# Optimization experiments

Measured on AMD Instinct MI355X. Metric: run time of the kernel, lower is better.

Reference implementation:

```python
import jax, jax.numpy as jnp
import numpy as np

SPATIAL_SHAPES = [(80, 80), (40, 40), (20, 20)]
NUM_POINTS = [4, 4, 4]
N_HEADS = 8
OFFSET_SCALE = 0.5
LN_EPS = 1e-5


def layer_norm(x, w, b):
    m = x.mean(-1, keepdims=True)
    v = ((x - m) ** 2).mean(-1, keepdims=True)
    return (x - m) * jax.lax.rsqrt(v + LN_EPS) * w + b


def grid_sample(img, grid):
    """Bilinear, zero padding, align_corners=False.
    img: [N, C, H, W], grid: [N, Q, P, 2] in [-1, 1] -> [N, C, Q, P]."""
    N, C, H, W = img.shape
    gx = (grid[..., 0] + 1.0) * (W * 0.5) - 0.5
    gy = (grid[..., 1] + 1.0) * (H * 0.5) - 0.5
    x0 = jnp.floor(gx)
    y0 = jnp.floor(gy)
    wx1 = gx - x0
    wy1 = gy - y0
    x0i = x0.astype(jnp.int32)
    y0i = y0.astype(jnp.int32)
    flat = img.reshape(N, C, H * W)
    Q, P = grid.shape[1], grid.shape[2]

    def corner(xi, yi, w):
        valid = (xi >= 0) & (xi < W) & (yi >= 0) & (yi < H)
        idx = jnp.clip(yi, 0, H - 1) * W + jnp.clip(xi, 0, W - 1)
        v = jnp.take_along_axis(flat, idx.reshape(N, 1, Q * P), axis=2)
        v = v.reshape(N, C, Q, P)
        return v * (w * valid.astype(w.dtype))[:, None]

    return (corner(x0i, y0i, (1 - wx1) * (1 - wy1))
            + corner(x0i + 1, y0i, wx1 * (1 - wy1))
            + corner(x0i, y0i + 1, (1 - wx1) * wy1)
            + corner(x0i + 1, y0i + 1, wx1 * wy1))


def setup_inputs() -> dict:
    key = jax.random.key(0)
    ks = iter(jax.random.split(key, 40))
    B, Q, D, FF = 32, 300, 256, 1024
    S = sum(h * w for h, w in SPATIAL_SHAPES)  # 8400
    SP = sum(NUM_POINTS)  # 12

    def w(shape, scale=0.02):
        return jax.random.normal(next(ks), shape, jnp.float32) * scale

    inp = {
        'hidden_states': jax.random.normal(next(ks), (B, Q, D), jnp.float32),
        'position_embeddings': jax.random.normal(next(ks), (B, Q, D), jnp.float32),
        'reference_points': jax.random.uniform(next(ks), (B, Q, 1, 4), jnp.float32),
        'encoder_hidden_states': jax.random.normal(next(ks), (B, S, D), jnp.float32),
        'q_w': w((D, D)), 'q_b': jnp.zeros((D,), jnp.float32),
        'k_w': w((D, D)), 'k_b': jnp.zeros((D,), jnp.float32),
        'v_w': w((D, D)), 'v_b': jnp.zeros((D,), jnp.float32),
        'o_w': w((D, D)), 'o_b': jnp.zeros((D,), jnp.float32),
        'sa_ln_w': jnp.ones((D,), jnp.float32), 'sa_ln_b': jnp.zeros((D,), jnp.float32),
        'off_w': w((D, N_HEADS * SP * 2)), 'off_b': w((N_HEADS * SP * 2,), 0.1),
        'aw_w': w((D, N_HEADS * SP)), 'aw_b': jnp.zeros((N_HEADS * SP,), jnp.float32),
        'gate_w': w((2 * D, 2 * D)), 'gate_b': jnp.zeros((2 * D,), jnp.float32),
        'gate_ln_w': jnp.ones((D,), jnp.float32), 'gate_ln_b': jnp.zeros((D,), jnp.float32),
        'fc1_w': w((D, FF)), 'fc1_b': jnp.zeros((FF,), jnp.float32),
        'fc2_w': w((FF, D)), 'fc2_b': jnp.zeros((D,), jnp.float32),
        'fin_ln_w': jnp.ones((D,), jnp.float32), 'fin_ln_b': jnp.zeros((D,), jnp.float32),
    }
    return inp


def reference(hidden_states, position_embeddings, reference_points, encoder_hidden_states,
              q_w, q_b, k_w, k_b, v_w, v_b, o_w, o_b, sa_ln_w, sa_ln_b,
              off_w, off_b, aw_w, aw_b, gate_w, gate_b, gate_ln_w, gate_ln_b,
              fc1_w, fc1_b, fc2_w, fc2_b, fin_ln_w, fin_ln_b):
    B, Q, D = hidden_states.shape
    H = N_HEADS
    hd = D // H
    scaling = hd ** -0.5

    # ---- self attention (queries attend to queries, pos added to q/k only) ----
    hq = hidden_states + position_embeddings
    q = ((hq @ q_w + q_b) * scaling).reshape(B, Q, H, hd)
    k = (hq @ k_w + k_b).reshape(B, Q, H, hd)
    v = (hidden_states @ v_w + v_b).reshape(B, Q, H, hd)
    attn = jax.nn.softmax(jnp.einsum('bqhd,bkhd->bhqk', q, k), axis=-1)
    sa = jnp.einsum('bhqk,bkhd->bqhd', attn, v).reshape(B, Q, D) @ o_w + o_b
    hidden_states = layer_norm(hidden_states + sa, sa_ln_w, sa_ln_b)
    second_residual = hidden_states

    # ---- multi-scale deformable cross attention ----
    S = encoder_hidden_states.shape[1]
    SP = sum(NUM_POINTS)
    value = encoder_hidden_states.reshape(B, S, H, hd)
    offs = (hidden_states @ off_w + off_b).reshape(B, Q, H, SP, 2)
    aw = jax.nn.softmax((hidden_states @ aw_w + aw_b).reshape(B, Q, H, SP), axis=-1)
    nps = jnp.asarray([1.0 / n for n in NUM_POINTS for _ in range(n)], hidden_states.dtype)
    offset = offs * nps[:, None] * reference_points[:, :, None, :, 2:] * OFFSET_SCALE
    loc = reference_points[:, :, None, :, :2] + offset          # [B,Q,H,SP,2]
    grids = (2.0 * loc - 1.0).transpose(0, 2, 1, 3, 4).reshape(B * H, Q, SP, 2)
    val = value.transpose(0, 2, 3, 1).reshape(B * H, hd, S)

    sampled = []
    s0, p0 = 0, 0
    for (hl, wl), pl in zip(SPATIAL_SHAPES, NUM_POINTS):
        v_l = val[:, :, s0:s0 + hl * wl].reshape(B * H, hd, hl, wl)
        sampled.append(grid_sample(v_l, grids[:, :, p0:p0 + pl]))
        s0 += hl * wl
        p0 += pl
    sampled = jnp.concatenate(sampled, axis=-1)                 # [B*H,hd,Q,SP]
    aw = aw.transpose(0, 2, 1, 3).reshape(B * H, 1, Q, SP)
    ca = (sampled * aw).sum(-1).reshape(B, D, Q).transpose(0, 2, 1)

    # ---- gated residual ----
    gates = jax.nn.sigmoid(jnp.concatenate([second_residual, ca], -1) @ gate_w + gate_b)
    g1, g2 = gates[..., :D], gates[..., D:]
    hidden_states = layer_norm(g1 * second_residual + g2 * ca, gate_ln_w, gate_ln_b)

    # ---- FFN ----
    ffn = jax.nn.relu(hidden_states @ fc1_w + fc1_b) @ fc2_w + fc2_b
    return layer_norm(hidden_states + ffn, fin_ln_w, fin_ln_b)
```

## Files before the change

kernel.cpp:

```cpp
#include <hip/hip_runtime.h>
#include <cmath>

#define BQ 300
#define DIM 256
#define NH 8
#define HD 32
#define NB 32
#define MROWS 9600
#define SENC 8400

typedef unsigned short ushort_t;
typedef __attribute__((ext_vector_type(8))) short short8;
typedef __attribute__((ext_vector_type(4))) float f32x4;
typedef __attribute__((ext_vector_type(4))) unsigned short us4;

__device__ __forceinline__ float bf2f(ushort_t u) {
    union { unsigned u32; float f; } x; x.u32 = ((unsigned)u) << 16; return x.f;
}
__device__ __forceinline__ ushort_t f2bf(float f) {
    union { float f; unsigned u; } x; x.f = f;
    unsigned u = x.u;
    u += 0x7fffu + ((u >> 16) & 1u);
    return (ushort_t)(u >> 16);
}

__global__ __launch_bounds__(256)
void wtrans_all(const float* __restrict__ q_w, const float* __restrict__ k_w,
                const float* __restrict__ v_w, const float* __restrict__ o_w,
                const float* __restrict__ off_w, const float* __restrict__ aw_w,
                const float* __restrict__ gate_w, const float* __restrict__ fc1_w,
                const float* __restrict__ fc2_w,
                ushort_t* __restrict__ qkT, ushort_t* __restrict__ vT,
                ushort_t* __restrict__ oT, ushort_t* __restrict__ offawT,
                ushort_t* __restrict__ gT, ushort_t* __restrict__ f1T,
                ushort_t* __restrict__ f2T,
                const float* __restrict__ q_b, float* __restrict__ qsb,
                float scal)
{
    __shared__ float t[32][33];
    const int bid = blockIdx.x;
    const float* src; ushort_t* dst; int K, N, local; float scale = 1.0f;

    if (bid < 64)       { src = q_w;   dst = qkT;             K = 256; N = 256;  local = bid;       scale = scal; }
    else if (bid < 128) { src = k_w;   dst = qkT + 256 * 256; K = 256; N = 256;  local = bid - 64; }
    else if (bid < 192) { src = v_w;   dst = vT;              K = 256; N = 256;  local = bid - 128; }
    else if (bid < 256) { src = o_w;   dst = oT;              K = 256; N = 256;  local = bid - 192; }
    else if (bid < 304) { src = off_w; dst = offawT;          K = 256; N = 192;  local = bid - 256; }
    else if (bid < 328) { src = aw_w;  dst = offawT + 192 * 256; K = 256; N = 96; local = bid - 304; }
    else if (bid < 336) {
        int l = bid - 328;
        ushort_t* d2 = offawT + 288 * 256 + l * 32;
        for (int e = threadIdx.x; e < 32 * 32; e += 256) { int r = e >> 5, c = e & 31; d2[r * 256 + c] = 0; }
        return;
    }
    else if (bid < 592) { src = gate_w; dst = gT;  K = 512;  N = 512;  local = bid - 336; }
    else if (bid < 848) { src = fc1_w;  dst = f1T; K = 256;  N = 1024; local = bid - 592; }
    else if (bid < 1104){ src = fc2_w;  dst = f2T; K = 1024; N = 256;  local = bid - 848; }
    else {
        if (threadIdx.x < 256) qsb[threadIdx.x] = q_b[threadIdx.x] * scal;
        return;
    }
    const int tilesx = N >> 5;
    const int n0 = (local % tilesx) * 32, k0 = (local / tilesx) * 32;
    const int tx = threadIdx.x & 31, ty = threadIdx.x >> 5;
    #pragma unroll
    for (int i = 0; i < 4; ++i)
        t[ty + i * 8][tx] = src[(size_t)(k0 + ty + i * 8) * N + n0 + tx];
    __syncthreads();
    #pragma unroll
    for (int i = 0; i < 4; ++i)
        dst[(size_t)(n0 + ty + i * 8) * K + k0 + tx] = f2bf(t[tx][ty + i * 8] * scale);
}

__global__ __launch_bounds__(256)
void cvt2(const float* __restrict__ hidden, const float* __restrict__ pos,
          ushort_t* __restrict__ hq, ushort_t* __restrict__ hid)
{
    int i = blockIdx.x * 256 + threadIdx.x;
    if (i < 614400) {
        float4 a = ((const float4*)hidden)[i];
        float4 b = ((const float4*)pos)[i];
        us4 u;
        u.x = f2bf(a.x + b.x); u.y = f2bf(a.y + b.y);
        u.z = f2bf(a.z + b.z); u.w = f2bf(a.w + b.w);
        *(us4*)&hq[(size_t)i * 4] = u;
    } else {
        i -= 614400;
        float4 a = ((const float4*)hidden)[i];
        us4 u;
        u.x = f2bf(a.x); u.y = f2bf(a.y); u.z = f2bf(a.z); u.w = f2bf(a.w);
        *(us4*)&hid[(size_t)i * 4] = u;
    }
}

template<int BM, int BN, int ACT, bool OBF>
__global__ __launch_bounds__(256)
void gemm_mfma(const ushort_t* __restrict__ A, int lda,
               const ushort_t* __restrict__ Bt, int K,
               const float* __restrict__ bias, const float* __restrict__ bias2,
               int bsplit, int N,
               float* __restrict__ Cf, ushort_t* __restrict__ Cb, int ldc)
{
    constexpr int LDT = 40;
    __shared__ ushort_t As[BM * LDT];
    __shared__ ushort_t Bs[BN * LDT];
    const int tid = threadIdx.x;
    const int row0 = blockIdx.y * BM, col0 = blockIdx.x * BN;
    const int lane = tid & 63, wid = tid >> 6;
    const int wm = wid >> 1, wn = wid & 1;
    constexpr int FM = BM / 32, FN = BN / 32;
    const int r16 = lane & 15, kg = lane >> 4;

    f32x4 acc[FM][FN];
    #pragma unroll
    for (int m = 0; m < FM; ++m)
        #pragma unroll
        for (int n = 0; n < FN; ++n) {
            f32x4 z = {0.f, 0.f, 0.f, 0.f};
            acc[m][n] = z;
        }

    for (int k0 = 0; k0 < K; k0 += 32) {
        #pragma unroll
        for (int c = 0; c < BM * 4 / 256; ++c) {
            int idx = tid + c * 256;
            int r = idx >> 2, cc = idx & 3;
            *(short8*)&As[r * LDT + cc * 8] =
                *(const short8*)&A[(size_t)(row0 + r) * lda + k0 + cc * 8];
        }
        #pragma unroll
        for (int c = 0; c < BN * 4 / 256; ++c) {
            int idx = tid + c * 256;
            int r = idx >> 2, cc = idx & 3;
            *(short8*)&Bs[r * LDT + cc * 8] =
                *(const short8*)&Bt[(size_t)(col0 + r) * K + k0 + cc * 8];
        }
        __syncthreads();
        short8 a[FM], b[FN];
        #pragma unroll
        for (int m = 0; m < FM; ++m)
            a[m] = *(const short8*)&As[(wm * (BM / 2) + m * 16 + r16) * LDT + kg * 8];
        #pragma unroll
        for (int n = 0; n < FN; ++n)
            b[n] = *(const short8*)&Bs[(wn * (BN / 2) + n * 16 + r16) * LDT + kg * 8];
        #pragma unroll
        for (int m = 0; m < FM; ++m)
            #pragma unroll
            for (int n = 0; n < FN; ++n)
                acc[m][n] = __builtin_amdgcn_mfma_f32_16x16x32_bf16(a[m], b[n], acc[m][n], 0, 0, 0);
        __syncthreads();
    }

    #pragma unroll
    for (int m = 0; m < FM; ++m) {
        #pragma unroll
        for (int n = 0; n < FN; ++n) {
            int colb = col0 + wn * (BN / 2) + n * 16 + r16;
            float bs;
            if (colb < bsplit) bs = bias[colb];
            else if (colb < N) bs = bias2[colb - bsplit];
            else bs = 0.0f;
            #pragma unroll
            for (int r = 0; r < 4; ++r) {
                int row = row0 + wm * (BM / 2) + m * 16 + kg * 4 + r;
                float v = acc[m][n][r] + bs;
                if (ACT == 1) v = fmaxf(v, 0.0f);
                if (ACT == 2) v = 1.0f / (1.0f + __expf(-v));
                if (OBF) Cb[(size_t)row * ldc + colb] = f2bf(v);
                else     Cf[(size_t)row * ldc + colb] = v;
            }
        }
    }
}

__global__ __launch_bounds__(256)
void attn_flash(const ushort_t* __restrict__ QK, const ushort_t* __restrict__ V,
                ushort_t* __restrict__ O)
{
    __shared__ ushort_t ks[64 * 40];
    __shared__ ushort_t vt[32 * 72];
    __shared__ float    ss[32 * 68];
    __shared__ ushort_t ps[32 * 72];
    __shared__ float    ml[32], ll[32], fl[32];

    const int orig = blockIdx.x;
    const int wg = (orig & 7) * 320 + (orig >> 3);
    const int qc = wg % 10, bh = wg / 10;
    const int b = bh >> 3, h = bh & 7;
    const int q0 = qc * 32;
    const int nq = (BQ - q0 < 32) ? (BQ - q0) : 32;

    const int tid = threadIdx.x;
    const int lane = tid & 63, wid = tid >> 6;
    const int r16 = lane & 15, kg = lane >> 4;
    const int wm = wid >> 1, wn = wid & 1;

    if (tid < 32) { ml[tid] = -1e30f; ll[tid] = 0.f; }

    short8 aq[2];
    #pragma unroll
    for (int rt = 0; rt < 2; ++rt) {
        int qr = q0 + rt * 16 + r16;
        if (qr > BQ - 1) qr = BQ - 1;
        aq[rt] = *(const short8*)&QK[((size_t)(b * BQ + qr)) * 512 + h * 32 + kg * 8];
    }
    f32x4 oacc = {0.f, 0.f, 0.f, 0.f};

    for (int kt = 0; kt < 5; ++kt) {
        __syncthreads();
        {
            int kk = tid >> 2, c8 = (tid & 3) * 8;
            int ki = kt * 64 + kk;
            short8 kv = {0, 0, 0, 0, 0, 0, 0, 0};
            short8 vv = {0, 0, 0, 0, 0, 0, 0, 0};
            if (ki < BQ) {
                kv = *(const short8*)&QK[((size_t)(b * BQ + ki)) * 512 + 256 + h * 32 + c8];
                vv = *(const short8*)&V[((size_t)(b * BQ + ki)) * 256 + h * 32 + c8];
            }
            *(short8*)&ks[kk * 40 + c8] = kv;
            #pragma unroll
            for (int j = 0; j < 8; ++j) vt[(c8 + j) * 72 + kk] = (ushort_t)vv[j];
        }
        __syncthreads();
        {
            short8 bk = *(const short8*)&ks[(wid * 16 + r16) * 40 + kg * 8];
            #pragma unroll
            for (int rt = 0; rt < 2; ++rt) {
                f32x4 sacc = {0.f, 0.f, 0.f, 0.f};
                sacc = __builtin_amdgcn_mfma_f32_16x16x32_bf16(aq[rt], bk, sacc, 0, 0, 0);
                #pragma unroll
                for (int r = 0; r < 4; ++r)
                    ss[(rt * 16 + kg * 4 + r) * 68 + wid * 16 + r16] = sacc[r];
            }
        }
        __syncthreads();
        #pragma unroll
        for (int j = 0; j < 8; ++j) {
            int row = wid * 8 + j;
            float s = ss[row * 68 + lane];
            if (kt * 64 + lane >= BQ) s = -1e30f;
            float tm = s;
            #pragma unroll
            for (int off = 32; off; off >>= 1) tm = fmaxf(tm, __shfl_xor(tm, off));
            float mold = ml[row];
            float mnew = fmaxf(mold, tm);
            float p = __expf(s - mnew);
            float psum = p;
            #pragma unroll
            for (int off = 32; off; off >>= 1) psum += __shfl_xor(psum, off);
            if (lane == 0) {
                float f = __expf(mold - mnew);
                ml[row] = mnew;
                ll[row] = ll[row] * f + psum;
                fl[row] = f;
            }
            ps[row * 72 + lane] = f2bf(p);
        }
        __syncthreads();
        {
            #pragma unroll
            for (int r = 0; r < 4; ++r)
                oacc[r] *= fl[wm * 16 + kg * 4 + r];
            #pragma unroll
            for (int kstep = 0; kstep < 2; ++kstep) {
                short8 pa = *(const short8*)&ps[(wm * 16 + r16) * 72 + kstep * 32 + kg * 8];
                short8 bv = *(const short8*)&vt[(wn * 16 + r16) * 72 + kstep * 32 + kg * 8];
                oacc = __builtin_amdgcn_mfma_f32_16x16x32_bf16(pa, bv, oacc, 0, 0, 0);
            }
        }
    }
    __syncthreads();
    #pragma unroll
    for (int r = 0; r < 4; ++r) {
        int rowl = wm * 16 + kg * 4 + r;
        if (rowl < nq) {
            float v = oacc[r] / ll[rowl];
            O[((size_t)(b * BQ + q0 + rowl)) * 256 + h * 32 + wn * 16 + r16] = f2bf(v);
        }
    }
}

__global__ __launch_bounds__(256)
void ln_add(const float* __restrict__ X, const float* __restrict__ Y,
            const float* __restrict__ w, const float* __restrict__ b,
            float* __restrict__ outf, ushort_t* __restrict__ outbf, int ldbf)
{
    const int row = blockIdx.x * 4 + (threadIdx.x >> 6);
    const int lane = threadIdx.x & 63;
    float v[4];
    #pragma unroll
    for (int i = 0; i < 4; ++i) {
        int c = lane + 64 * i;
        v[i] = X[(size_t)row * DIM + c] + Y[(size_t)row * DIM + c];
    }
    float s = v[0] + v[1] + v[2] + v[3];
    float s2 = v[0]*v[0] + v[1]*v[1] + v[2]*v[2] + v[3]*v[3];
    #pragma unroll
    for (int off = 32; off; off >>= 1) { s += __shfl_xor(s, off); s2 += __shfl_xor(s2, off); }
    const float mean = s * (1.0f / DIM);
    const float var = s2 * (1.0f / DIM) - mean * mean;
    const float inv = rsqrtf(var + 1e-5f);
    #pragma unroll
    for (int i = 0; i < 4; ++i) {
        int c = lane + 64 * i;
        float r = (v[i] - mean) * inv * w[c] + b[c];
        if (outf)  outf[(size_t)row * DIM + c] = r;
        if (outbf) outbf[(size_t)row * ldbf + c] = f2bf(r);
    }
}

__global__ __launch_bounds__(256)
void ln_gate(const ushort_t* __restrict__ C2, const ushort_t* __restrict__ G,
             const float* __restrict__ w, const float* __restrict__ b,
             float* __restrict__ outf, ushort_t* __restrict__ outbf)
{
    const int row = blockIdx.x * 4 + (threadIdx.x >> 6);
    const int lane = threadIdx.x & 63;
    float v[4];
    #pragma unroll
    for (int i = 0; i < 4; ++i) {
        int c = lane + 64 * i;
        float h1 = bf2f(C2[(size_t)row * 512 + c]);
        float ca = bf2f(C2[(size_t)row * 512 + 256 + c]);
        float g1 = bf2f(G[(size_t)row * 512 + c]);
        float g2 = bf2f(G[(size_t)row * 512 + 256 + c]);
        v[i] = g1 * h1 + g2 * ca;
    }
    float s = v[0] + v[1] + v[2] + v[3];
    float s2 = v[0]*v[0] + v[1]*v[1] + v[2]*v[2] + v[3]*v[3];
    #pragma unroll
    for (int off = 32; off; off >>= 1) { s += __shfl_xor(s, off); s2 += __shfl_xor(s2, off); }
    const float mean = s * (1.0f / DIM);
    const float var = s2 * (1.0f / DIM) - mean * mean;
    const float inv = rsqrtf(var + 1e-5f);
    #pragma unroll
    for (int i = 0; i < 4; ++i) {
        int c = lane + 64 * i;
        float r = (v[i] - mean) * inv * w[c] + b[c];
        outf[(size_t)row * DIM + c] = r;
        outbf[(size_t)row * DIM + c] = f2bf(r);
    }
}

__global__ __launch_bounds__(256)
void sample_kernel(const float* __restrict__ enc, const float* __restrict__ offaw,
                   const float* __restrict__ ref, ushort_t* __restrict__ C2out)
{
    __shared__ float sofs[4][320];
    __shared__ float sref[4][4];

    const int orig = blockIdx.x;
    const int blk = (orig & 7) * 300 + (orig >> 3);
    const int b = blk / 75;
    const int q0 = (blk % 75) * 4;
    const int tid = threadIdx.x;
    const int qq = tid >> 6;
    const int h = (tid >> 3) & 7;
    const int d4 = tid & 7;
    const int bq = b * BQ + q0 + qq;

    for (int e = tid; e < 4 * 80; e += 256) {
        int row = e >> 6 >= 0 ? e / 80 : 0, c4 = e % 80;
        row = e / 80;
        ((float4*)&sofs[row][0])[c4] =
            ((const float4*)(offaw + (size_t)(b * BQ + q0 + row) * 320))[c4];
    }
    if (tid < 16)
        sref[tid >> 2][tid & 3] = ref[(size_t)(b * BQ + q0 + (tid >> 2)) * 4 + (tid & 3)];
    __syncthreads();

    const float rx = sref[qq][0], ry = sref[qq][1];
    const float rw = sref[qq][2], rh = sref[qq][3];
    const float* op = &sofs[qq][h * 24];
    const float* ap = &sofs[qq][192 + h * 12];

    float wgt[12];
    float mx = -1e30f;
    #pragma unroll
    for (int j = 0; j < 12; ++j) { wgt[j] = ap[j]; mx = fmaxf(mx, wgt[j]); }
    float sum = 0.0f;
    #pragma unroll
    for (int j = 0; j < 12; ++j) { wgt[j] = __expf(wgt[j] - mx); sum += wgt[j]; }
    const float isum = 1.0f / sum;

    f32x4 acc = {0.f, 0.f, 0.f, 0.f};
    int p = 0;
    #pragma unroll
    for (int l = 0; l < 3; ++l) {
        const int Wl = (l == 0) ? 80 : (l == 1 ? 40 : 20);
        const int Hl = Wl;
        const int soff = (l == 0) ? 0 : (l == 1 ? 6400 : 8000);
        const float* base = enc + ((size_t)(b * SENC + soff)) * DIM + h * HD + d4 * 4;
        #pragma unroll
        for (int pp = 0; pp < 4; ++pp, ++p) {
            const float ox = op[p * 2 + 0], oy = op[p * 2 + 1];
            const float lx = rx + ox * 0.25f * rw * 0.5f;
            const float ly = ry + oy * 0.25f * rh * 0.5f;
            const float gx = lx * (float)Wl - 0.5f;
            const float gy = ly * (float)Hl - 0.5f;
            const float x0f = floorf(gx), y0f = floorf(gy);
            const int x0 = (int)x0f, y0 = (int)y0f;
            const float wx1 = gx - x0f, wy1 = gy - y0f;
            const float wx0 = 1.0f - wx1, wy0 = 1.0f - wy1;
            const bool vx0 = (x0 >= 0) & (x0 < Wl);
            const bool vx1 = (x0 + 1 >= 0) & (x0 + 1 < Wl);
            const bool vy0 = (y0 >= 0) & (y0 < Hl);
            const bool vy1 = (y0 + 1 >= 0) & (y0 + 1 < Hl);
            const int xc0 = min(max(x0, 0), Wl - 1);
            const int xc1 = min(max(x0 + 1, 0), Wl - 1);
            const int yc0 = min(max(y0, 0), Hl - 1);
            const int yc1 = min(max(y0 + 1, 0), Hl - 1);
            const float aw2 = wgt[p] * isum;
            const float w00 = wx0 * wy0 * ((vx0 & vy0) ? aw2 : 0.0f);
            const float w10 = wx1 * wy0 * ((vx1 & vy0) ? aw2 : 0.0f);
            const float w01 = wx0 * wy1 * ((vx0 & vy1) ? aw2 : 0.0f);
            const float w11 = wx1 * wy1 * ((vx1 & vy1) ? aw2 : 0.0f);
            f32x4 c00 = *(const f32x4*)&base[((size_t)(yc0 * Wl + xc0)) * DIM];
            f32x4 c10 = *(const f32x4*)&base[((size_t)(yc0 * Wl + xc1)) * DIM];
            f32x4 c01 = *(const f32x4*)&base[((size_t)(yc1 * Wl + xc0)) * DIM];
            f32x4 c11 = *(const f32x4*)&base[((size_t)(yc1 * Wl + xc1)) * DIM];
            #pragma unroll
            for (int r = 0; r < 4; ++r)
                acc[r] += w00 * c00[r] + w10 * c10[r] + w01 * c01[r] + w11 * c11[r];
        }
    }
    us4 u;
    u.x = f2bf(acc[0]); u.y = f2bf(acc[1]); u.z = f2bf(acc[2]); u.w = f2bf(acc[3]);
    *(us4*)&C2out[(size_t)bq * 512 + 256 + h * HD + d4 * 4] = u;
}

extern "C" void kernel_launch(void* const* d_in, const int* in_sizes, int n_in,
                              void* d_out, int out_size, void* d_ws, size_t ws_size,
                              hipStream_t stream)
{
    (void)in_sizes; (void)n_in; (void)out_size; (void)ws_size;
    const float* hidden   = (const float*)d_in[0];
    const float* pos      = (const float*)d_in[1];
    const float* ref      = (const float*)d_in[2];
    const float* enc      = (const float*)d_in[3];
    const float* q_w      = (const float*)d_in[4];
    const float* q_b      = (const float*)d_in[5];
    const float* k_w      = (const float*)d_in[6];
    const float* k_b      = (const float*)d_in[7];
    const float* v_w      = (const float*)d_in[8];
    const float* v_b      = (const float*)d_in[9];
    const float* o_w      = (const float*)d_in[10];
    const float* o_b      = (const float*)d_in[11];
    const float* sa_ln_w  = (const float*)d_in[12];
    const float* sa_ln_b  = (const float*)d_in[13];
    const float* off_w    = (const float*)d_in[14];
    const float* off_b    = (const float*)d_in[15];
    const float* aw_w     = (const float*)d_in[16];
    const float* aw_b     = (const float*)d_in[17];
    const float* gate_w   = (const float*)d_in[18];
    const float* gate_b   = (const float*)d_in[19];
    const float* gate_ln_w= (const float*)d_in[20];
    const float* gate_ln_b= (const float*)d_in[21];
    const float* fc1_w    = (const float*)d_in[22];
    const float* fc1_b    = (const float*)d_in[23];
    const float* fc2_w    = (const float*)d_in[24];
    const float* fc2_b    = (const float*)d_in[25];
    const float* fin_ln_w = (const float*)d_in[26];
    const float* fin_ln_b = (const float*)d_in[27];
    float* out = (float*)d_out;

    char* wsb = (char*)d_ws;
    ushort_t* hqbf   = (ushort_t*)(wsb + 0);
    ushort_t* hidbf  = (ushort_t*)(wsb + 4915200);
    ushort_t* QKbuf  = (ushort_t*)(wsb + 9830400);
    ushort_t* Vbf    = (ushort_t*)(wsb + 19660800);
    ushort_t* aobf   = (ushort_t*)(wsb + 24576000);
    float*    SA     = (float*)(wsb + 0);
    ushort_t* C2     = (ushort_t*)(wsb + 9830400);
    float*    offaw  = (float*)(wsb + 19660800);
    ushort_t* gatesbf= (ushort_t*)(wsb + 0);
    ushort_t* midbf  = (ushort_t*)(wsb + 19660800);
    float*    ffn    = (float*)(wsb + 0);
    ushort_t* h2bf   = (ushort_t*)(wsb + 39321600);
    ushort_t* qkT    = (ushort_t*)(wsb + 44236800);
    ushort_t* vT     = (ushort_t*)(wsb + 44498944);
    ushort_t* oT     = (ushort_t*)(wsb + 44630016);
    ushort_t* offawT = (ushort_t*)(wsb + 44761088);
    ushort_t* gT     = (ushort_t*)(wsb + 44924928);
    ushort_t* f1T    = (ushort_t*)(wsb + 45449216);
    ushort_t* f2T    = (ushort_t*)(wsb + 45973504);
    float*    qsb    = (float*)(wsb + 46497792);

    const dim3 blk(256);
    const float scal = 0.17677669529663687f;

    wtrans_all<<<dim3(1105), blk, 0, stream>>>(q_w, k_w, v_w, o_w, off_w, aw_w,
                                               gate_w, fc1_w, fc2_w,
                                               qkT, vT, oT, offawT, gT, f1T, f2T,
                                               q_b, qsb, scal);
    cvt2<<<dim3(4800), blk, 0, stream>>>(hidden, pos, hqbf, hidbf);

    gemm_mfma<128,128,0,true><<<dim3(4,75), blk, 0, stream>>>(hqbf, 256, qkT, 256, qsb, k_b, 256, 512, nullptr, QKbuf, 512);
    gemm_mfma<128,128,0,true><<<dim3(2,75), blk, 0, stream>>>(hidbf, 256, vT, 256, v_b, nullptr, 256, 256, nullptr, Vbf, 256);

    attn_flash<<<dim3(2560), blk, 0, stream>>>(QKbuf, Vbf, aobf);

    gemm_mfma<128,128,0,false><<<dim3(2,75), blk, 0, stream>>>(aobf, 256, oT, 256, o_b, nullptr, 256, 256, SA, nullptr, 256);
    ln_add<<<dim3(2400), blk, 0, stream>>>(SA, hidden, sa_ln_w, sa_ln_b, nullptr, C2, 512);

    gemm_mfma<128,64,0,false><<<dim3(5,75), blk, 0, stream>>>(C2, 512, offawT, 256, off_b, aw_b, 192, 288, offaw, nullptr, 320);

    sample_kernel<<<dim3(2400), blk, 0, stream>>>(enc, offaw, ref, C2);

    gemm_mfma<128,128,2,true><<<dim3(4,75), blk, 0, stream>>>(C2, 512, gT, 512, gate_b, nullptr, 512, 512, nullptr, gatesbf, 512);
    ln_gate<<<dim3(2400), blk, 0, stream>>>(C2, gatesbf, gate_ln_w, gate_ln_b, out, h2bf);

    gemm_mfma<128,128,1,true><<<dim3(8,75), blk, 0, stream>>>(h2bf, 256, f1T, 256, fc1_b, nullptr, 1024, 1024, nullptr, midbf, 1024);
    gemm_mfma<128,128,0,false><<<dim3(2,75), blk, 0, stream>>>(midbf, 1024, f2T, 1024, fc2_b, nullptr, 256, 256, ffn, nullptr, 256);
    ln_add<<<dim3(2400), blk, 0, stream>>>(ffn, out, fin_ln_w, fin_ln_b, out, nullptr, 0);
}
```

Before: 269.1 us.

## Enlarge attention query tile to 64 and precompute sampling indices in shared memory

The flash attention kernel now handles 64 queries per block instead of 32. Each wave owns a 16-row query tile and computes scores across all four key sub-tiles, which halves the grid and halves how often K and V are reloaded from global memory. The deformable sampling kernel now computes the softmax, bilinear weights and corner indices once per (query, head, point) into shared memory, then gathers from that table. Previously the softmax and coordinate math was repeated by all 8 lanes that share a head. The trade-off is more shared memory per block in both kernels, with possible occupancy loss, plus an extra barrier in the sampler.

New measurement: 277.9 us. 1.03x slower.

```diff
diff --git a/kernel.cpp b/kernel.cpp
--- a/kernel.cpp
+++ b/kernel.cpp
@@ -179,32 +179,34 @@
 {
     __shared__ ushort_t ks[64 * 40];
     __shared__ ushort_t vt[32 * 72];
-    __shared__ float    ss[32 * 68];
-    __shared__ ushort_t ps[32 * 72];
-    __shared__ float    ml[32], ll[32], fl[32];
+    __shared__ float    ss[64 * 68];
+    __shared__ ushort_t ps[64 * 72];
+    __shared__ float    ml[64], ll[64], fl[64];
 
     const int orig = blockIdx.x;
-    const int wg = (orig & 7) * 320 + (orig >> 3);
-    const int qc = wg % 10, bh = wg / 10;
+    const int wg = (orig & 7) * 160 + (orig >> 3);
+    const int qc = wg % 5, bh = wg / 5;
     const int b = bh >> 3, h = bh & 7;
-    const int q0 = qc * 32;
-    const int nq = (BQ - q0 < 32) ? (BQ - q0) : 32;
+    const int q0 = qc * 64;
+    const int nq = (BQ - q0 < 64) ? (BQ - q0) : 64;
 
     const int tid = threadIdx.x;
     const int lane = tid & 63, wid = tid >> 6;
     const int r16 = lane & 15, kg = lane >> 4;
-    const int wm = wid >> 1, wn = wid & 1;
-
-    if (tid < 32) { ml[tid] = -1e30f; ll[tid] = 0.f; }
-
-    short8 aq[2];
-    #pragma unroll
-    for (int rt = 0; rt < 2; ++rt) {
-        int qr = q0 + rt * 16 + r16;
+
+    if (tid < 64) { ml[tid] = -1e30f; ll[tid] = 0.f; }
+
+    short8 aq;
+    {
+        int qr = q0 + wid * 16 + r16;
         if (qr > BQ - 1) qr = BQ - 1;
-        aq[rt] = *(const short8*)&QK[((size_t)(b * BQ + qr)) * 512 + h * 32 + kg * 8];
-    }
-    f32x4 oacc = {0.f, 0.f, 0.f, 0.f};
+        aq = *(const short8*)&QK[((size_t)(b * BQ + qr)) * 512 + h * 32 + kg * 8];
+    }
+    f32x4 oacc[2];
+    {
+        f32x4 z = {0.f, 0.f, 0.f, 0.f};
+        oacc[0] = z; oacc[1] = z;
+    }
 
     for (int kt = 0; kt < 5; ++kt) {
         __syncthreads();
@@ -222,21 +224,19 @@
             for (int j = 0; j < 8; ++j) vt[(c8 + j) * 72 + kk] = (ushort_t)vv[j];
         }
         __syncthreads();
-        {
-            short8 bk = *(const short8*)&ks[(wid * 16 + r16) * 40 + kg * 8];
-            #pragma unroll
-            for (int rt = 0; rt < 2; ++rt) {
-                f32x4 sacc = {0.f, 0.f, 0.f, 0.f};
-                sacc = __builtin_amdgcn_mfma_f32_16x16x32_bf16(aq[rt], bk, sacc, 0, 0, 0);
-                #pragma unroll
-                for (int r = 0; r < 4; ++r)
-                    ss[(rt * 16 + kg * 4 + r) * 68 + wid * 16 + r16] = sacc[r];
-            }
+        #pragma unroll
+        for (int ktile = 0; ktile < 4; ++ktile) {
+            short8 bk = *(const short8*)&ks[(ktile * 16 + r16) * 40 + kg * 8];
+            f32x4 sacc = {0.f, 0.f, 0.f, 0.f};
+            sacc = __builtin_amdgcn_mfma_f32_16x16x32_bf16(aq, bk, sacc, 0, 0, 0);
+            #pragma unroll
+            for (int r = 0; r < 4; ++r)
+                ss[(wid * 16 + kg * 4 + r) * 68 + ktile * 16 + r16] = sacc[r];
         }
         __syncthreads();
         #pragma unroll
-        for (int j = 0; j < 8; ++j) {
-            int row = wid * 8 + j;
+        for (int j = 0; j < 16; ++j) {
+            int row = wid * 16 + j;
             float s = ss[row * 68 + lane];
             if (kt * 64 + lane >= BQ) s = -1e30f;
             float tm = s;
@@ -259,25 +259,31 @@
         __syncthreads();
         {
             #pragma unroll
-            for (int r = 0; r < 4; ++r)
-                oacc[r] *= fl[wm * 16 + kg * 4 + r];
-            #pragma unroll
-            for (int kstep = 0; kstep < 2; ++kstep) {
-                short8 pa = *(const short8*)&ps[(wm * 16 + r16) * 72 + kstep * 32 + kg * 8];
-                short8 bv = *(const short8*)&vt[(wn * 16 + r16) * 72 + kstep * 32 + kg * 8];
-                oacc = __builtin_amdgcn_mfma_f32_16x16x32_bf16(pa, bv, oacc, 0, 0, 0);
+            for (int r = 0; r < 4; ++r) {
+                float f = fl[wid * 16 + kg * 4 + r];
+                oacc[0][r] *= f; oacc[1][r] *= f;
             }
+            #pragma unroll
+            for (int nt = 0; nt < 2; ++nt)
+                #pragma unroll
+                for (int kstep = 0; kstep < 2; ++kstep) {
+                    short8 pa = *(const short8*)&ps[(wid * 16 + r16) * 72 + kstep * 32 + kg * 8];
+                    short8 bv = *(const short8*)&vt[(nt * 16 + r16) * 72 + kstep * 32 + kg * 8];
+                    oacc[nt] = __builtin_amdgcn_mfma_f32_16x16x32_bf16(pa, bv, oacc[nt], 0, 0, 0);
+                }
         }
     }
     __syncthreads();
     #pragma unroll
-    for (int r = 0; r < 4; ++r) {
-        int rowl = wm * 16 + kg * 4 + r;
-        if (rowl < nq) {
-            float v = oacc[r] / ll[rowl];
-            O[((size_t)(b * BQ + q0 + rowl)) * 256 + h * 32 + wn * 16 + r16] = f2bf(v);
-        }
-    }
+    for (int nt = 0; nt < 2; ++nt)
+        #pragma unroll
+        for (int r = 0; r < 4; ++r) {
+            int rowl = wid * 16 + kg * 4 + r;
+            if (rowl < nq) {
+                float v = oacc[nt][r] / ll[rowl];
+                O[((size_t)(b * BQ + q0 + rowl)) * 256 + h * 32 + nt * 16 + r16] = f2bf(v);
+            }
+        }
 }
 
 __global__ __launch_bounds__(256)
@@ -347,86 +353,90 @@
                    const float* __restrict__ ref, ushort_t* __restrict__ C2out)
 {
     __shared__ float sofs[4][320];
-    __shared__ float sref[4][4];
+    __shared__ float sref[16];
+    __shared__ float swgt[384][5];
+    __shared__ int   sidx[384][5];
 
     const int orig = blockIdx.x;
     const int blk = (orig & 7) * 300 + (orig >> 3);
     const int b = blk / 75;
     const int q0 = (blk % 75) * 4;
     const int tid = threadIdx.x;
-    const int qq = tid >> 6;
-    const int h = (tid >> 3) & 7;
-    const int d4 = tid & 7;
-    const int bq = b * BQ + q0 + qq;
 
     for (int e = tid; e < 4 * 80; e += 256) {
-        int row = e >> 6 >= 0 ? e / 80 : 0, c4 = e % 80;
-        row = e / 80;
+        int row = e / 80, c4 = e % 80;
         ((float4*)&sofs[row][0])[c4] =
             ((const float4*)(offaw + (size_t)(b * BQ + q0 + row) * 320))[c4];
     }
     if (tid < 16)
-        sref[tid >> 2][tid & 3] = ref[(size_t)(b * BQ + q0 + (tid >> 2)) * 4 + (tid & 3)];
+        sref[tid] = ref[(size_t)(b * BQ + q0 + (tid >> 2)) * 4 + (tid & 3)];
     __syncthreads();
 
-    const float rx = sref[qq][0], ry = sref[qq][1];
-    const float rw = sref[qq][2], rh = sref[qq][3];
-    const float* op = &sofs[qq][h * 24];
-    const float* ap = &sofs[qq][192 + h * 12];
-
-    float wgt[12];
-    float mx = -1e30f;
-    #pragma unroll
-    for (int j = 0; j < 12; ++j) { wgt[j] = ap[j]; mx = fmaxf(mx, wgt[j]); }
-    float sum = 0.0f;
-    #pragma unroll
-    for (int j = 0; j < 12; ++j) { wgt[j] = __expf(wgt[j] - mx); sum += wgt[j]; }
-    const float isum = 1.0f / sum;
-
+    for (int it = tid; it < 384; it += 256) {
+        const int qq = it / 96, rem = it % 96;
+        const int h = rem / 12, p = rem % 12;
+        const float* ap = &sofs[qq][192 + h * 12];
+        float mx = -1e30f;
+        #pragma unroll
+        for (int j = 0; j < 12; ++j) mx = fmaxf(mx, ap[j]);
+        float sum = 0.0f;
+        #pragma unroll
+        for (int j = 0; j < 12; ++j) sum += __expf(ap[j] - mx);
+        const float aw2 = __expf(ap[p] - mx) / sum;
+
+        const int l = p >> 2;
+        const int Wl = (l == 0) ? 80 : (l == 1 ? 40 : 20);
+        const int soff = (l == 0) ? 0 : (l == 1 ? 6400 : 8000);
+        const float rx = sref[qq * 4 + 0], ry = sref[qq * 4 + 1];
+        const float rw = sref[qq * 4 + 2], rh = sref[qq * 4 + 3];
+        const float ox = sofs[qq][h * 24 + p * 2], oy = sofs[qq][h * 24 + p * 2 + 1];
+        const float gx = (rx + ox * 0.125f * rw) * (float)Wl - 0.5f;
+        const float gy = (ry + oy * 0.125f * rh) * (float)Wl - 0.5f;
+        const float x0f = floorf(gx), y0f = floorf(gy);
+        const int x0 = (int)x0f, y0 = (int)y0f;
+        const float wx1 = gx - x0f, wy1 = gy - y0f;
+        const float wx0 = 1.0f - wx1, wy0 = 1.0f - wy1;
+        const bool vx0 = (x0 >= 0) & (x0 < Wl);
+        const bool vx1 = (x0 + 1 >= 0) & (x0 + 1 < Wl);
+        const bool vy0 = (y0 >= 0) & (y0 < Wl);
+        const bool vy1 = (y0 + 1 >= 0) & (y0 + 1 < Wl);
+        const int xc0 = min(max(x0, 0), Wl - 1);
+        const int xc1 = min(max(x0 + 1, 0), Wl - 1);
+        const int yc0 = min(max(y0, 0), Wl - 1);
+        const int yc1 = min(max(y0 + 1, 0), Wl - 1);
+        swgt[it][0] = wx0 * wy0 * ((vx0 & vy0) ? aw2 : 0.0f);
+        swgt[it][1] = wx1 * wy0 * ((vx1 & vy0) ? aw2 : 0.0f);
+        swgt[it][2] = wx0 * wy1 * ((vx0 & vy1) ? aw2 : 0.0f);
+        swgt[it][3] = wx1 * wy1 * ((vx1 & vy1) ? aw2 : 0.0f);
+        sidx[it][0] = (soff + yc0 * Wl + xc0) * 256;
+        sidx[it][1] = (soff + yc0 * Wl + xc1) * 256;
+        sidx[it][2] = (soff + yc1 * Wl + xc0) * 256;
+        sidx[it][3] = (soff + yc1 * Wl + xc1) * 256;
+    }
+    __syncthreads();
+
+    const int qq = tid >> 6, h = (tid >> 3) & 7, d4 = tid & 7;
+    const float* basebd = enc + (size_t)b * SENC * 256 + h * 32 + d4 * 4;
     f32x4 acc = {0.f, 0.f, 0.f, 0.f};
-    int p = 0;
-    #pragma unroll
-    for (int l = 0; l < 3; ++l) {
-        const int Wl = (l == 0) ? 80 : (l == 1 ? 40 : 20);
-        const int Hl = Wl;
-        const int soff = (l == 0) ? 0 : (l == 1 ? 6400 : 8000);
-        const float* base = enc + ((size_t)(b * SENC + soff)) * DIM + h * HD + d4 * 4;
-        #pragma unroll
-        for (int pp = 0; pp < 4; ++pp, ++p) {
-            const float ox = op[p * 2 + 0], oy = op[p * 2 + 1];
-            const float lx = rx + ox * 0.25f * rw * 0.5f;
-            const float ly = ry + oy * 0.25f * rh * 0.5f;
-            const float gx = lx * (float)Wl - 0.5f;
-            const float gy = ly * (float)Hl - 0.5f;
-            const float x0f = floorf(gx), y0f = floorf(gy);
-            const int x0 = (int)x0f, y0 = (int)y0f;
-            const float wx1 = gx - x0f, wy1 = gy - y0f;
-            const float wx0 = 1.0f - wx1, wy0 = 1.0f - wy1;
-            const bool vx0 = (x0 >= 0) & (x0 < Wl);
-            const bool vx1 = (x0 + 1 >= 0) & (x0 + 1 < Wl);
-            const bool vy0 = (y0 >= 0) & (y0 < Hl);
-            const bool vy1 = (y0 + 1 >= 0) & (y0 + 1 < Hl);
-            const int xc0 = min(max(x0, 0), Wl - 1);
-            const int xc1 = min(max(x0 + 1, 0), Wl - 1);
-            const int yc0 = min(max(y0, 0), Hl - 1);
-            const int yc1 = min(max(y0 + 1, 0), Hl - 1);
-            const float aw2 = wgt[p] * isum;
-            const float w00 = wx0 * wy0 * ((vx0 & vy0) ? aw2 : 0.0f);
-            const float w10 = wx1 * wy0 * ((vx1 & vy0) ? aw2 : 0.0f);
-            const float w01 = wx0 * wy1 * ((vx0 & vy1) ? aw2 : 0.0f);
-            const float w11 = wx1 * wy1 * ((vx1 & vy1) ? aw2 : 0.0f);
-            f32x4 c00 = *(const f32x4*)&base[((size_t)(yc0 * Wl + xc0)) * DIM];
-            f32x4 c10 = *(const f32x4*)&base[((size_t)(yc0 * Wl + xc1)) * DIM];
-            f32x4 c01 = *(const f32x4*)&base[((size_t)(yc1 * Wl + xc0)) * DIM];
-            f32x4 c11 = *(const f32x4*)&base[((size_t)(yc1 * Wl + xc1)) * DIM];
-            #pragma unroll
-            for (int r = 0; r < 4; ++r)
-                acc[r] += w00 * c00[r] + w10 * c10[r] + w01 * c01[r] + w11 * c11[r];
-        }
+    const int itb = qq * 96 + h * 12;
+    #pragma unroll
+    for (int p = 0; p < 12; ++p) {
+        const int it = itb + p;
+        const int i00 = sidx[it][0], i10 = sidx[it][1];
+        const int i01 = sidx[it][2], i11 = sidx[it][3];
+        const float w00 = swgt[it][0], w10 = swgt[it][1];
+        const float w01 = swgt[it][2], w11 = swgt[it][3];
+        f32x4 c00 = *(const f32x4*)&basebd[i00];
+        f32x4 c10 = *(const f32x4*)&basebd[i10];
+        f32x4 c01 = *(const f32x4*)&basebd[i01];
+        f32x4 c11 = *(const f32x4*)&basebd[i11];
+        #pragma unroll
+        for (int r = 0; r < 4; ++r)
+            acc[r] += w00 * c00[r] + w10 * c10[r] + w01 * c01[r] + w11 * c11[r];
     }
     us4 u;
     u.x = f2bf(acc[0]); u.y = f2bf(acc[1]); u.z = f2bf(acc[2]); u.w = f2bf(acc[3]);
-    *(us4*)&C2out[(size_t)bq * 512 + 256 + h * HD + d4 * 4] = u;
+    *(us4*)&C2out[(size_t)(b * BQ + q0 + qq) * 512 + 256 + h * HD + d4 * 4] = u;
 }
 
 extern "C" void kernel_launch(void* const* d_in, const int* in_sizes, int n_in,
@@ -498,7 +508,7 @@
     gemm_mfma<128,128,0,true><<<dim3(4,75), blk, 0, stream>>>(hqbf, 256, qkT, 256, qsb, k_b, 256, 512, nullptr, QKbuf, 512);
     gemm_mfma<128,128,0,true><<<dim3(2,75), blk, 0, stream>>>(hidbf, 256, vT, 256, v_b, nullptr, 256, 256, nullptr, Vbf, 256);
 
-    attn_flash<<<dim3(2560), blk, 0, stream>>>(QKbuf, Vbf, aobf);
+    attn_flash<<<dim3(1280), blk, 0, stream>>>(QKbuf, Vbf, aobf);
 
     gemm_mfma<128,128,0,false><<<dim3(2,75), blk, 0, stream>>>(aobf, 256, oT, 256, o_b, nullptr, 256, 256, SA, nullptr, 256);
     ln_add<<<dim3(2400), blk, 0, stream>>>(SA, hidden, sa_ln_w, sa_ln_b, nullptr, C2, 512);
```

## Fuse prep kernels, merge QK and V projections, shrink GEMM tiles for occupancy

Applied to the files above, without the earlier changes.

Merges the weight-transpose and activation-conversion kernels into one launch. Combines the QK and V projection GEMMs into a single 768-wide GEMM that picks its A operand per column block, writing one interleaved QKV buffer that attention reads. Shrinks tile sizes on several small-N GEMMs to 64x64 or 64x128 so more workgroups fill the GPU. This cuts launch count and tail effects, at the cost of less data reuse per tile and a wider row stride in attention loads.

Result: faster. 243.5 us (-9.5%).

```diff
diff --git a/kernel.cpp b/kernel.cpp
--- a/kernel.cpp
+++ b/kernel.cpp
@@ -25,44 +25,70 @@
 }
 
 __global__ __launch_bounds__(256)
-void wtrans_all(const float* __restrict__ q_w, const float* __restrict__ k_w,
-                const float* __restrict__ v_w, const float* __restrict__ o_w,
-                const float* __restrict__ off_w, const float* __restrict__ aw_w,
-                const float* __restrict__ gate_w, const float* __restrict__ fc1_w,
-                const float* __restrict__ fc2_w,
-                ushort_t* __restrict__ qkT, ushort_t* __restrict__ vT,
-                ushort_t* __restrict__ oT, ushort_t* __restrict__ offawT,
-                ushort_t* __restrict__ gT, ushort_t* __restrict__ f1T,
-                ushort_t* __restrict__ f2T,
-                const float* __restrict__ q_b, float* __restrict__ qsb,
-                float scal)
-{
+void prep_all(const float* __restrict__ hidden, const float* __restrict__ pos,
+              ushort_t* __restrict__ hq, ushort_t* __restrict__ hid,
+              const float* __restrict__ q_w, const float* __restrict__ k_w,
+              const float* __restrict__ v_w, const float* __restrict__ o_w,
+              const float* __restrict__ off_w, const float* __restrict__ aw_w,
+              const float* __restrict__ gate_w, const float* __restrict__ fc1_w,
+              const float* __restrict__ fc2_w,
+              ushort_t* __restrict__ qkvT, ushort_t* __restrict__ oT,
+              ushort_t* __restrict__ offawT, ushort_t* __restrict__ gT,
+              ushort_t* __restrict__ f1T, ushort_t* __restrict__ f2T,
+              const float* __restrict__ q_b, const float* __restrict__ k_b,
+              const float* __restrict__ v_b, float* __restrict__ qkvb,
+              float scal)
+{
+    const int tid = threadIdx.x;
+    if (blockIdx.x < 4800) {
+        int i = blockIdx.x * 256 + tid;
+        if (i < 614400) {
+            float4 a = ((const float4*)hidden)[i];
+            float4 b = ((const float4*)pos)[i];
+            us4 u;
+            u.x = f2bf(a.x + b.x); u.y = f2bf(a.y + b.y);
+            u.z = f2bf(a.z + b.z); u.w = f2bf(a.w + b.w);
+            *(us4*)&hq[(size_t)i * 4] = u;
+        } else {
+            i -= 614400;
+            float4 a = ((const float4*)hidden)[i];
+            us4 u;
+            u.x = f2bf(a.x); u.y = f2bf(a.y); u.z = f2bf(a.z); u.w = f2bf(a.w);
+            *(us4*)&hid[(size_t)i * 4] = u;
+        }
+        return;
+    }
     __shared__ float t[32][33];
-    const int bid = blockIdx.x;
+    const int bid = blockIdx.x - 4800;
     const float* src; ushort_t* dst; int K, N, local; float scale = 1.0f;
 
-    if (bid < 64)       { src = q_w;   dst = qkT;             K = 256; N = 256;  local = bid;       scale = scal; }
-    else if (bid < 128) { src = k_w;   dst = qkT + 256 * 256; K = 256; N = 256;  local = bid - 64; }
-    else if (bid < 192) { src = v_w;   dst = vT;              K = 256; N = 256;  local = bid - 128; }
-    else if (bid < 256) { src = o_w;   dst = oT;              K = 256; N = 256;  local = bid - 192; }
-    else if (bid < 304) { src = off_w; dst = offawT;          K = 256; N = 192;  local = bid - 256; }
+    if (bid < 64)       { src = q_w;   dst = qkvT;             K = 256; N = 256;  local = bid;       scale = scal; }
+    else if (bid < 128) { src = k_w;   dst = qkvT + 256 * 256; K = 256; N = 256;  local = bid - 64; }
+    else if (bid < 192) { src = v_w;   dst = qkvT + 512 * 256; K = 256; N = 256;  local = bid - 128; }
+    else if (bid < 256) { src = o_w;   dst = oT;               K = 256; N = 256;  local = bid - 192; }
+    else if (bid < 304) { src = off_w; dst = offawT;           K = 256; N = 192;  local = bid - 256; }
     else if (bid < 328) { src = aw_w;  dst = offawT + 192 * 256; K = 256; N = 96; local = bid - 304; }
     else if (bid < 336) {
         int l = bid - 328;
         ushort_t* d2 = offawT + 288 * 256 + l * 32;
-        for (int e = threadIdx.x; e < 32 * 32; e += 256) { int r = e >> 5, c = e & 31; d2[r * 256 + c] = 0; }
+        for (int e = tid; e < 32 * 32; e += 256) { int r = e >> 5, c = e & 31; d2[r * 256 + c] = 0; }
         return;
     }
     else if (bid < 592) { src = gate_w; dst = gT;  K = 512;  N = 512;  local = bid - 336; }
     else if (bid < 848) { src = fc1_w;  dst = f1T; K = 256;  N = 1024; local = bid - 592; }
     else if (bid < 1104){ src = fc2_w;  dst = f2T; K = 1024; N = 256;  local = bid - 848; }
     else {
-        if (threadIdx.x < 256) qsb[threadIdx.x] = q_b[threadIdx.x] * scal;
+        #pragma unroll
+        for (int j = 0; j < 3; ++j) {
+            int c = j * 256 + tid;
+            float v = (j == 0) ? q_b[tid] * scal : (j == 1) ? k_b[tid] : v_b[tid];
+            qkvb[c] = v;
+        }
         return;
     }
     const int tilesx = N >> 5;
     const int n0 = (local % tilesx) * 32, k0 = (local / tilesx) * 32;
-    const int tx = threadIdx.x & 31, ty = threadIdx.x >> 5;
+    const int tx = tid & 31, ty = tid >> 5;
     #pragma unroll
     for (int i = 0; i < 4; ++i)
         t[ty + i * 8][tx] = src[(size_t)(k0 + ty + i * 8) * N + n0 + tx];
@@ -72,30 +98,10 @@
         dst[(size_t)(n0 + ty + i * 8) * K + k0 + tx] = f2bf(t[tx][ty + i * 8] * scale);
 }
 
-__global__ __launch_bounds__(256)
-void cvt2(const float* __restrict__ hidden, const float* __restrict__ pos,
-          ushort_t* __restrict__ hq, ushort_t* __restrict__ hid)
-{
-    int i = blockIdx.x * 256 + threadIdx.x;
-    if (i < 614400) {
-        float4 a = ((const float4*)hidden)[i];
-        float4 b = ((const float4*)pos)[i];
-        us4 u;
-        u.x = f2bf(a.x + b.x); u.y = f2bf(a.y + b.y);
-        u.z = f2bf(a.z + b.z); u.w = f2bf(a.w + b.w);
-        *(us4*)&hq[(size_t)i * 4] = u;
-    } else {
-        i -= 614400;
-        float4 a = ((const float4*)hidden)[i];
-        us4 u;
-        u.x = f2bf(a.x); u.y = f2bf(a.y); u.z = f2bf(a.z); u.w = f2bf(a.w);
-        *(us4*)&hid[(size_t)i * 4] = u;
-    }
-}
-
 template<int BM, int BN, int ACT, bool OBF>
 __global__ __launch_bounds__(256)
-void gemm_mfma(const ushort_t* __restrict__ A, int lda,
+void gemm_mfma(const ushort_t* __restrict__ A1, const ushort_t* __restrict__ A2,
+               int asplit, int lda,
                const ushort_t* __restrict__ Bt, int K,
                const float* __restrict__ bias, const float* __restrict__ bias2,
                int bsplit, int N,
@@ -106,6 +112,7 @@
     __shared__ ushort_t Bs[BN * LDT];
     const int tid = threadIdx.x;
     const int row0 = blockIdx.y * BM, col0 = blockIdx.x * BN;
+    const ushort_t* __restrict__ A = (col0 < asplit) ? A1 : A2;
     const int lane = tid & 63, wid = tid >> 6;
     const int wm = wid >> 1, wn = wid & 1;
     constexpr int FM = BM / 32, FN = BN / 32;
@@ -174,8 +181,7 @@
 }
 
 __global__ __launch_bounds__(256)
-void attn_flash(const ushort_t* __restrict__ QK, const ushort_t* __restrict__ V,
-                ushort_t* __restrict__ O)
+void attn_flash(const ushort_t* __restrict__ QKV, ushort_t* __restrict__ O)
 {
     __shared__ ushort_t ks[64 * 40];
     __shared__ ushort_t vt[32 * 72];
@@ -202,7 +208,7 @@
     for (int rt = 0; rt < 2; ++rt) {
         int qr = q0 + rt * 16 + r16;
         if (qr > BQ - 1) qr = BQ - 1;
-        aq[rt] = *(const short8*)&QK[((size_t)(b * BQ + qr)) * 512 + h * 32 + kg * 8];
+        aq[rt] = *(const short8*)&QKV[((size_t)(b * BQ + qr)) * 768 + h * 32 + kg * 8];
     }
     f32x4 oacc = {0.f, 0.f, 0.f, 0.f};
 
@@ -214,8 +220,9 @@
             short8 kv = {0, 0, 0, 0, 0, 0, 0, 0};
             short8 vv = {0, 0, 0, 0, 0, 0, 0, 0};
             if (ki < BQ) {
-                kv = *(const short8*)&QK[((size_t)(b * BQ + ki)) * 512 + 256 + h * 32 + c8];
-                vv = *(const short8*)&V[((size_t)(b * BQ + ki)) * 256 + h * 32 + c8];
+                size_t gi = ((size_t)(b * BQ + ki)) * 768 + h * 32 + c8;
+                kv = *(const short8*)&QKV[gi + 256];
+                vv = *(const short8*)&QKV[gi + 512];
             }
             *(short8*)&ks[kk * 40 + c8] = kv;
             #pragma unroll
@@ -360,8 +367,7 @@
     const int bq = b * BQ + q0 + qq;
 
     for (int e = tid; e < 4 * 80; e += 256) {
-        int row = e >> 6 >= 0 ? e / 80 : 0, c4 = e % 80;
-        row = e / 80;
+        int row = e / 80, c4 = e % 80;
         ((float4*)&sofs[row][0])[c4] =
             ((const float4*)(offaw + (size_t)(b * BQ + q0 + row) * 320))[c4];
     }
@@ -467,8 +473,7 @@
     char* wsb = (char*)d_ws;
     ushort_t* hqbf   = (ushort_t*)(wsb + 0);
     ushort_t* hidbf  = (ushort_t*)(wsb + 4915200);
-    ushort_t* QKbuf  = (ushort_t*)(wsb + 9830400);
-    ushort_t* Vbf    = (ushort_t*)(wsb + 19660800);
+    ushort_t* QKV    = (ushort_t*)(wsb + 9830400);
     ushort_t* aobf   = (ushort_t*)(wsb + 24576000);
     float*    SA     = (float*)(wsb + 0);
     ushort_t* C2     = (ushort_t*)(wsb + 9830400);
@@ -477,40 +482,39 @@
     ushort_t* midbf  = (ushort_t*)(wsb + 19660800);
     float*    ffn    = (float*)(wsb + 0);
     ushort_t* h2bf   = (ushort_t*)(wsb + 39321600);
-    ushort_t* qkT    = (ushort_t*)(wsb + 44236800);
-    ushort_t* vT     = (ushort_t*)(wsb + 44498944);
+    ushort_t* qkvT   = (ushort_t*)(wsb + 44236800);
     ushort_t* oT     = (ushort_t*)(wsb + 44630016);
     ushort_t* offawT = (ushort_t*)(wsb + 44761088);
     ushort_t* gT     = (ushort_t*)(wsb + 44924928);
     ushort_t* f1T    = (ushort_t*)(wsb + 45449216);
     ushort_t* f2T    = (ushort_t*)(wsb + 45973504);
-    float*    qsb    = (float*)(wsb + 46497792);
+    float*    qkvb   = (float*)(wsb + 46497792);
 
     const dim3 blk(256);
     const float scal = 0.17677669529663687f;
-
-    wtrans_all<<<dim3(1105), blk, 0, stream>>>(q_w, k_w, v_w, o_w, off_w, aw_w,
-                                               gate_w, fc1_w, fc2_w,
-                                               qkT, vT, oT, offawT, gT, f1T, f2T,
-                                               q_b, qsb, scal);
-    cvt2<<<dim3(4800), blk, 0, stream>>>(hidden, pos, hqbf, hidbf);
-
-    gemm_mfma<128,128,0,true><<<dim3(4,75), blk, 0, stream>>>(hqbf, 256, qkT, 256, qsb, k_b, 256, 512, nullptr, QKbuf, 512);
-    gemm_mfma<128,128,0,true><<<dim3(2,75), blk, 0, stream>>>(hidbf, 256, vT, 256, v_b, nullptr, 256, 256, nullptr, Vbf, 256);
-
-    attn_flash<<<dim3(2560), blk, 0, stream>>>(QKbuf, Vbf, aobf);
-
-    gemm_mfma<128,128,0,false><<<dim3(2,75), blk, 0, stream>>>(aobf, 256, oT, 256, o_b, nullptr, 256, 256, SA, nullptr, 256);
+    const int BIG = 1 << 30;
+
+    prep_all<<<dim3(5905), blk, 0, stream>>>(hidden, pos, hqbf, hidbf,
+                                             q_w, k_w, v_w, o_w, off_w, aw_w,
+                                             gate_w, fc1_w, fc2_w,
+                                             qkvT, oT, offawT, gT, f1T, f2T,
+                                             q_b, k_b, v_b, qkvb, scal);
+
+    gemm_mfma<64,128,0,true><<<dim3(6,150), blk, 0, stream>>>(hqbf, hidbf, 512, 256, qkvT, 256, qkvb, nullptr, 768, 768, nullptr, QKV, 768);
+
+    attn_flash<<<dim3(2560), blk, 0, stream>>>(QKV, aobf);
+
+    gemm_mfma<64,64,0,false><<<dim3(4,150), blk, 0, stream>>>(aobf, nullptr, BIG, 256, oT, 256, o_b, nullptr, 256, 256, SA, nullptr, 256);
     ln_add<<<dim3(2400), blk, 0, stream>>>(SA, hidden, sa_ln_w, sa_ln_b, nullptr, C2, 512);
 
-    gemm_mfma<128,64,0,false><<<dim3(5,75), blk, 0, stream>>>(C2, 512, offawT, 256, off_b, aw_b, 192, 288, offaw, nullptr, 320);
+    gemm_mfma<64,64,0,false><<<dim3(5,150), blk, 0, stream>>>(C2, nullptr, BIG, 512, offawT, 256, off_b, aw_b, 192, 288, offaw, nullptr, 320);
 
     sample_kernel<<<dim3(2400), blk, 0, stream>>>(enc, offaw, ref, C2);
 
-    gemm_mfma<128,128,2,true><<<dim3(4,75), blk, 0, stream>>>(C2, 512, gT, 512, gate_b, nullptr, 512, 512, nullptr, gatesbf, 512);
+    gemm_mfma<64,128,2,true><<<dim3(4,150), blk, 0, stream>>>(C2, nullptr, BIG, 512, gT, 512, gate_b, nullptr, 512, 512, nullptr, gatesbf, 512);
     ln_gate<<<dim3(2400), blk, 0, stream>>>(C2, gatesbf, gate_ln_w, gate_ln_b, out, h2bf);
 
-    gemm_mfma<128,128,1,true><<<dim3(8,75), blk, 0, stream>>>(h2bf, 256, f1T, 256, fc1_b, nullptr, 1024, 1024, nullptr, midbf, 1024);
-    gemm_mfma<128,128,0,false><<<dim3(2,75), blk, 0, stream>>>(midbf, 1024, f2T, 1024, fc2_b, nullptr, 256, 256, ffn, nullptr, 256);
+    gemm_mfma<128,128,1,true><<<dim3(8,75), blk, 0, stream>>>(h2bf, nullptr, BIG, 256, f1T, 256, fc1_b, nullptr, 1024, 1024, nullptr, midbf, 1024);
+    gemm_mfma<64,64,0,false><<<dim3(4,150), blk, 0, stream>>>(midbf, nullptr, BIG, 1024, f2T, 1024, fc2_b, nullptr, 256, 256, ffn, nullptr, 256);
     ln_add<<<dim3(2400), blk, 0, stream>>>(ffn, out, fin_ln_w, fin_ln_b, out, nullptr, 0);
 }
```
